# Performance work log

Measured on AMD Instinct MI355X. Metric: run time of the kernel, lower is better.

Reference implementation:

```python
import jax, jax.numpy as jnp
import numpy as np

L = 8        # path length (number of visited nodes)
N = 32768    # neighbors per node (fixed fan-out)
H = 404      # relation_dim == GRU hidden size
D = 128      # node_encode_dim
F = 532      # neighbor feature = D + H
SCALE = 0.05


def setup_inputs() -> dict:
    key = jax.random.key(0)
    ks = jax.random.split(key, 14)
    return {
        "query": jax.random.normal(ks[0], (1, H), jnp.float32),
        "path_nodes": jax.random.normal(ks[1], (L, D), jnp.float32),
        "neighbors": jax.random.normal(ks[2], (L, N, F), jnp.float32),
        "action_ids": jax.random.randint(ks[3], (L - 1,), 0, N),
        "W_ih": jax.random.normal(ks[4], (3 * H, 3 * D), jnp.float32) * SCALE,
        "W_hh": jax.random.normal(ks[5], (3 * H, H), jnp.float32) * SCALE,
        "b_ih": jax.random.normal(ks[6], (3 * H,), jnp.float32) * SCALE,
        "b_hh": jax.random.normal(ks[7], (3 * H,), jnp.float32) * SCALE,
        "W_fa": jax.random.normal(ks[8], (D, F), jnp.float32) * SCALE,
        "b_fa": jax.random.normal(ks[9], (D,), jnp.float32) * SCALE,
        "W_fs": jax.random.normal(ks[10], (D, H), jnp.float32) * SCALE,
        "b_fs": jax.random.normal(ks[11], (D,), jnp.float32) * SCALE,
        "W_fp": jax.random.normal(ks[12], (1, 2 * D), jnp.float32) * SCALE,
        "b_fp": jax.random.normal(ks[13], (1,), jnp.float32) * SCALE,
    }


def gru_cell(x, h, W_ih, W_hh, b_ih, b_hh):
    # torch.nn.GRUCell semantics; x: (1, 3D), h: (1, H)
    gi = x @ W_ih.T + b_ih   # (1, 3H)
    gh = h @ W_hh.T + b_hh   # (1, 3H)
    i_r, i_z, i_n = jnp.split(gi, 3, axis=-1)
    h_r, h_z, h_n = jnp.split(gh, 3, axis=-1)
    r = jax.nn.sigmoid(i_r + h_r)
    z = jax.nn.sigmoid(i_z + h_z)
    n = jnp.tanh(i_n + r * h_n)
    return (1.0 - z) * n + z * h


def reference(query, path_nodes, neighbors, action_ids,
              W_ih, W_hh, b_ih, b_hh, W_fa, b_fa, W_fs, b_fs, W_fp, b_fp):
    # FA over all hops' neighbor blocks at once: (L, N, F) x (D, F) -> (L, N, D)
    hnts = jnp.einsum('lnf,df->lnd', neighbors, W_fa) + b_fa
    hmax = jnp.max(hnts, axis=1)                        # (L, D)  column-wise max (== _Max)
    hsel = hnts[jnp.arange(L - 1), action_ids]          # (L-1, D) chosen-action rows

    # initial GRU step: cat(zeros, zeros, first node emb) with query as hidden
    x0 = jnp.concatenate([jnp.zeros((1, 2 * D), query.dtype), path_nodes[0:1]], axis=1)
    qt = gru_cell(x0, query, W_ih, W_hh, b_ih, b_hh)

    def step(qt, inp):
        hAt, hat, nxt = inp                             # each (D,)
        x = jnp.concatenate([hAt, hat, nxt])[None, :]   # (1, 3D)
        return gru_cell(x, qt, W_ih, W_hh, b_ih, b_hh), None

    qt, _ = jax.lax.scan(step, qt, (hmax[:-1], hsel, path_nodes[1:]))

    hSt = qt @ W_fs.T + b_fs                            # (1, D)
    u0 = jnp.concatenate([hSt, hmax[-1:]], axis=1) @ W_fp.T + b_fp   # (1, 1)
    uks = hSt @ hnts[-1].T                              # (1, N)
    return jax.nn.softmax(jnp.concatenate([u0, uks], axis=1), axis=1)
```

## Files before the change

kernel.cpp:

```cpp
#include <hip/hip_runtime.h>
#include <math.h>

#define L 8
#define N 32768
#define H 404
#define D 128
#define F 532
#define KT 9
#define GRU_BLOCKS 101

typedef __attribute__((ext_vector_type(8))) _Float16 half8;
typedef __attribute__((ext_vector_type(4))) float f32x4;
typedef __attribute__((address_space(3))) unsigned int as3_u32;
typedef __attribute__((address_space(1))) unsigned int as1_u32;

#define WS_WH2     0
#define WS_HMAXK   (WS_WH2 + 36864)
#define WS_HSEL    (WS_HMAXK + L * D)
#define WS_GI      (WS_HSEL + (L - 1) * D)
#define WS_HBUF    (WS_GI + L * 3 * H)
#define WS_HS      (WS_HBUF + 2 * H)
#define WS_SCAL    (WS_HS + D)
#define WS_CNT     (WS_SCAL + 4)
#define WS_PM      (WS_CNT + 4)
#define WS_PS      (WS_PM + 256)
#define WS_LOGITS  (WS_PS + 256)

__device__ __forceinline__ unsigned encf(float f) {
    unsigned u = __float_as_uint(f);
    return (u & 0x80000000u) ? ~u : (u | 0x80000000u);
}
__device__ __forceinline__ float decf(unsigned u) {
    unsigned b = (u & 0x80000000u) ? (u ^ 0x80000000u) : ~u;
    return __uint_as_float(b);
}
__device__ __forceinline__ float sigmoidf_(float x) {
    return 1.0f / (1.0f + __expf(-x));
}
__device__ __forceinline__ unsigned pk_f16(float a, float b) {
    auto h = __builtin_amdgcn_cvt_pkrtz(a, b);
    return *(unsigned*)&h;
}
__device__ __forceinline__ half8 pack8(float4 x0, float4 x1) {
    uint4 u = { pk_f16(x0.x, x0.y), pk_f16(x0.z, x0.w),
                pk_f16(x1.x, x1.y), pk_f16(x1.z, x1.w) };
    return *(half8*)&u;
}
__device__ __forceinline__ void gld16(const void* g, void* l) {
    __builtin_amdgcn_global_load_lds((const as1_u32*)g, (as3_u32*)l, 16, 0, 0);
}
__device__ __forceinline__ float aload(const float* p) {
    return __hip_atomic_load(p, __ATOMIC_RELAXED, __HIP_MEMORY_SCOPE_AGENT);
}
__device__ __forceinline__ void astore(float* p, float v) {
    __hip_atomic_store(p, v, __ATOMIC_RELAXED, __HIP_MEMORY_SCOPE_AGENT);
}

__global__ void k_prep(const float* __restrict__ Wfa, unsigned short* __restrict__ wh2,
                       unsigned* __restrict__ keys, unsigned* __restrict__ cnt) {
    int i = blockIdx.x * 256 + threadIdx.x;
    if (i < L * D) keys[i] = 0u;
    if (i == 2000) *cnt = 0u;
    if (i >= KT * 128 * 8) return;
    int kt = i / (128 * 8);
    int rem = i - kt * 128 * 8;
    int c = rem >> 3, j = rem & 7;
    int k0 = kt * 64 + (j ^ (c & 7)) * 8;
    unsigned short v[8];
#pragma unroll
    for (int e = 0; e < 8; ++e) {
        int k = k0 + e;
        float x = (k < F) ? Wfa[c * F + k] : 0.0f;
        _Float16 h = (_Float16)x;
        v[e] = *(unsigned short*)&h;
    }
    *(uint4*)(wh2 + (long)i * 8) = *(uint4*)v;
}

template<int HOP7>
__global__ __launch_bounds__(256, 3)
void k_big(const float* __restrict__ nb, const unsigned short* __restrict__ wh2,
           const float* __restrict__ bfa, const int* __restrict__ aid,
           unsigned* __restrict__ hmaxk, float* __restrict__ hsel,
           const float* __restrict__ hs_ws, float* __restrict__ logits,
           float* __restrict__ pm, float* __restrict__ ps) {
    __shared__ float As[128 * 64];
    __shared__ unsigned short Bs[128 * 64];
    __shared__ float sm2[2], ss2[2];

    const int bid = blockIdx.x;
    const int l_hop = HOP7 ? 7 : (bid >> 8);
    const int row0 = HOP7 ? bid * 128 : (bid & 255) * 128;
    const int tid = threadIdx.x;
    const int lane = tid & 63, w = tid >> 6;
    const int wm = w >> 1, wn = w & 1;
    const int lr = lane & 15, kg = lane >> 4;

    const float* xbase = nb + ((long)l_hop * N + row0) * F;

    f32x4 acc[4][4];
    float bv[4];
#pragma unroll
    for (int n = 0; n < 4; ++n) bv[n] = bfa[wn * 64 + n * 16 + lr];
#pragma unroll
    for (int m = 0; m < 4; ++m)
#pragma unroll
        for (int n = 0; n < 4; ++n) {
            acc[m][n][0] = bv[n]; acc[m][n][1] = bv[n];
            acc[m][n][2] = bv[n]; acc[m][n][3] = bv[n];
        }

    const int srow = lane >> 4;
    const int scp  = lane & 15;

    for (int kt = 0; kt < KT; ++kt) {
        const int fc = kt * 64;
        __syncthreads();
#pragma unroll
        for (int it = 0; it < 8; ++it) {
            int rbase = it * 16 + w * 4;
            int row = rbase + srow;
            int cg = scp ^ (row & 7);
            int col0 = fc + cg * 4;
            const float* src = xbase + (long)row * F + ((col0 < F) ? col0 : 0);
            gld16(src, (char*)As + rbase * 256);
        }
#pragma unroll
        for (int it = 0; it < 4; ++it) {
            int rb = it * 32 + w * 8;
            const char* src = (const char*)wh2 + (long)kt * 16384 + rb * 128 + lane * 16;
            gld16(src, (char*)Bs + rb * 128);
        }
        __syncthreads();

#pragma unroll
        for (int ks = 0; ks < 2; ++ks) {
            half8 b[4];
#pragma unroll
            for (int n = 0; n < 4; ++n) {
                int col = wn * 64 + n * 16 + lr;
                int ch = (ks * 4 + kg) ^ (col & 7);
                b[n] = *(const half8*)((const char*)Bs + col * 128 + ch * 16);
            }
#pragma unroll
            for (int m = 0; m < 4; ++m) {
                int row = wm * 64 + m * 16 + lr;
                int c0 = ks * 8 + kg * 2;
                const char* base = (const char*)As + row * 256;
                float4 x0 = *(const float4*)(base + (((c0)     ^ (row & 7)) << 4));
                float4 x1 = *(const float4*)(base + (((c0 + 1) ^ (row & 7)) << 4));
                half8 a = pack8(x0, x1);
#pragma unroll
                for (int n = 0; n < 4; ++n)
                    acc[m][n] = __builtin_amdgcn_mfma_f32_16x16x32_f16(a, b[n], acc[m][n], 0, 0, 0);
            }
        }
    }

    __syncthreads();

    if (!HOP7) {
        int br = aid[l_hop] - row0;
        if (br >= 0 && br < 128 && (br >> 6) == wm && ((br >> 2) & 3) == kg) {
            int msel = (br >> 4) & 3, rsel = br & 3;
#pragma unroll
            for (int n = 0; n < 4; ++n) {
                float vsel = 0.f;
#pragma unroll
                for (int m = 0; m < 4; ++m)
#pragma unroll
                    for (int r = 0; r < 4; ++r)
                        if (m == msel && r == rsel) vsel = acc[m][n][r];
                hsel[l_hop * D + wn * 64 + n * 16 + lr] = vsel;
            }
        }
    } else {
        float hsv[4];
#pragma unroll
        for (int n = 0; n < 4; ++n) hsv[n] = hs_ws[wn * 64 + n * 16 + lr];
        float p[4][4];
#pragma unroll
        for (int m = 0; m < 4; ++m)
#pragma unroll
            for (int r = 0; r < 4; ++r) {
                float s = hsv[0] * acc[m][0][r];
                s = fmaf(hsv[1], acc[m][1][r], s);
                s = fmaf(hsv[2], acc[m][2][r], s);
                s = fmaf(hsv[3], acc[m][3][r], s);
#pragma unroll
                for (int off = 1; off < 16; off <<= 1)
                    s += __shfl_xor(s, off, 64);
                p[m][r] = s;
            }
        float* part = (float*)As;
        if (lr == 0) {
#pragma unroll
            for (int m = 0; m < 4; ++m)
#pragma unroll
                for (int r = 0; r < 4; ++r)
                    part[wn * 128 + wm * 64 + m * 16 + kg * 4 + r] = p[m][r];
        }
        __syncthreads();
        float val = -3.4e38f, sv = 0.f;
        if (tid < 128) {
            val = part[tid] + part[128 + tid];
            logits[1 + row0 + tid] = val;
            sv = 1.0f;
        }
        float mv = val;
        for (int off = 1; off < 64; off <<= 1) {
            float m2 = __shfl_xor(mv, off, 64);
            float s2 = __shfl_xor(sv, off, 64);
            float M = fmaxf(mv, m2);
            sv = sv * __expf(mv - M) + s2 * __expf(m2 - M);
            mv = M;
        }
        if (lane == 0 && w < 2) { sm2[w] = mv; ss2[w] = sv; }
        __syncthreads();
        if (tid == 0) {
            float M = fmaxf(sm2[0], sm2[1]);
            float S = ss2[0] * __expf(sm2[0] - M) + ss2[1] * __expf(sm2[1] - M);
            pm[bid] = M; ps[bid] = S;
        }
        __syncthreads();
    }

    float cmax[4];
#pragma unroll
    for (int n = 0; n < 4; ++n) {
        float m0 = acc[0][n][0];
#pragma unroll
        for (int m = 0; m < 4; ++m)
#pragma unroll
            for (int r = 0; r < 4; ++r) m0 = fmaxf(m0, acc[m][n][r]);
        m0 = fmaxf(m0, __shfl_xor(m0, 16, 64));
        m0 = fmaxf(m0, __shfl_xor(m0, 32, 64));
        cmax[n] = m0;
    }
    float* wmaxp = (float*)As;
    if (kg == 0) {
#pragma unroll
        for (int n = 0; n < 4; ++n)
            wmaxp[wm * 128 + wn * 64 + n * 16 + lr] = cmax[n];
    }
    __syncthreads();
    if (tid < 128) {
        float mval = fmaxf(wmaxp[tid], wmaxp[128 + tid]);
        atomicMax(&hmaxk[l_hop * D + tid], encf(mval));
    }
}

__global__ void k_gi(const float* __restrict__ Wih, const float* __restrict__ bih,
                     const float* __restrict__ pn, const unsigned* __restrict__ hmaxk,
                     const float* __restrict__ hsel, float* __restrict__ gi) {
    __shared__ float xs[L][3 * D];
    const int tid = threadIdx.x;
    for (int i = tid; i < L * 3 * D; i += 256) {
        int t = i / (3 * D), k = i % (3 * D);
        float x;
        if (t == 0) {
            x = (k < 2 * D) ? 0.0f : pn[k - 2 * D];
        } else {
            if (k < D)            x = decf(hmaxk[(t - 1) * D + k]);
            else if (k < 2 * D)   x = hsel[(t - 1) * D + (k - D)];
            else                  x = pn[t * D + (k - 2 * D)];
        }
        xs[t][k] = x;
    }
    __syncthreads();

    const int lane = tid & 63;
    const int row = blockIdx.x * 4 + (tid >> 6);
    const float* wr = Wih + (long)row * 3 * D;
    float s[L];
#pragma unroll
    for (int t = 0; t < L; ++t) s[t] = 0.f;
#pragma unroll
    for (int c = 0; c < 6; ++c) {
        int k = lane + c * 64;
        float wv = wr[k];
#pragma unroll
        for (int t = 0; t < L; ++t) s[t] = fmaf(wv, xs[t][k], s[t]);
    }
#pragma unroll
    for (int t = 0; t < L; ++t)
        for (int off = 1; off < 64; off <<= 1) s[t] += __shfl_xor(s[t], off, 64);
    if (lane == 0) {
        float b = bih[row];
#pragma unroll
        for (int t = 0; t < L; ++t) gi[t * 3 * H + row] = s[t] + b;
    }
}

__global__ __launch_bounds__(256, 1)
void k_gru(const float* __restrict__ Whh, const float* __restrict__ bhh,
           const float* __restrict__ gi, const float* __restrict__ query,
           const float* __restrict__ Wfs, const float* __restrict__ bfs,
           float* __restrict__ hbuf, float* __restrict__ hs_ws,
           unsigned* __restrict__ cnt) {
    const int tid = threadIdx.x;
    const int lane = tid & 63;
    const int bid = blockIdx.x;
    const int j = bid * 4 + (tid >> 6);

    float wr[7], wz[7], wnn[7];
#pragma unroll
    for (int c = 0; c < 7; ++c) {
        int i = lane + c * 64;
        bool ok = i < H;
        wr[c]  = ok ? Whh[(long)j * H + i]           : 0.f;
        wz[c]  = ok ? Whh[(long)(H + j) * H + i]     : 0.f;
        wnn[c] = ok ? Whh[(long)(2 * H + j) * H + i] : 0.f;
    }
    float b_r = 0.f, b_z = 0.f, b_n = 0.f;
    if (lane == 0) { b_r = bhh[j]; b_z = bhh[H + j]; b_n = bhh[2 * H + j]; }

    for (int t = 0; t < L; ++t) {
        const float* hin = (t == 0) ? query : (hbuf + ((t - 1) & 1) * H);
        float* hout = hbuf + (t & 1) * H;
        float pr = 0.f, pz = 0.f, pn2 = 0.f;
#pragma unroll
        for (int c = 0; c < 7; ++c) {
            int i = lane + c * 64;
            float hv = 0.f;
            if (i < H) hv = (t == 0) ? hin[i] : aload(hin + i);
            pr  = fmaf(wr[c],  hv, pr);
            pz  = fmaf(wz[c],  hv, pz);
            pn2 = fmaf(wnn[c], hv, pn2);
        }
        for (int off = 1; off < 64; off <<= 1) {
            pr  += __shfl_xor(pr, off, 64);
            pz  += __shfl_xor(pz, off, 64);
            pn2 += __shfl_xor(pn2, off, 64);
        }
        if (lane == 0) {
            const float* gt = gi + t * 3 * H;
            float hprev = (t == 0) ? hin[j] : aload(hin + j);
            float r  = sigmoidf_(gt[j] + pr + b_r);
            float z  = sigmoidf_(gt[H + j] + pz + b_z);
            float nn = tanhf(gt[2 * H + j] + r * (pn2 + b_n));
            astore(hout + j, (1.0f - z) * nn + z * hprev);
        }
        __syncthreads();
        if (tid == 0) {
            __hip_atomic_fetch_add(cnt, 1u, __ATOMIC_RELEASE,
                                   __HIP_MEMORY_SCOPE_AGENT);
            unsigned target = (unsigned)GRU_BLOCKS * (t + 1);
            while (__hip_atomic_load(cnt, __ATOMIC_ACQUIRE,
                                     __HIP_MEMORY_SCOPE_AGENT) < target)
                __builtin_amdgcn_s_sleep(2);
        }
        __syncthreads();
    }

    if (bid < 32) {
        const float* qt = hbuf + H;
        int d = bid * 4 + (tid >> 6);
        float s = 0.f;
#pragma unroll
        for (int c = 0; c < 7; ++c) {
            int i = lane + c * 64;
            if (i < H) s = fmaf(aload(qt + i), Wfs[(long)d * H + i], s);
        }
        for (int off = 1; off < 64; off <<= 1) s += __shfl_xor(s, off, 64);
        if (lane == 0) astore(&hs_ws[d], s + bfs[d]);
    }
}

__global__ void k_sm12(const float* __restrict__ hs_ws, const float* __restrict__ Wfp,
                       const float* __restrict__ bfp, const unsigned* __restrict__ hmaxk,
                       const float* __restrict__ pm, const float* __restrict__ ps,
                       float* __restrict__ logits, float* __restrict__ scal) {
    __shared__ float red[4], reds[4], u0sh;
    int tid = threadIdx.x, lane = tid & 63, wid = tid >> 6;
    if (tid < 64) {
        float s = hs_ws[tid] * Wfp[tid];
        s = fmaf(hs_ws[tid + 64], Wfp[tid + 64], s);
        s = fmaf(decf(hmaxk[(L - 1) * D + tid]),      Wfp[D + tid],      s);
        s = fmaf(decf(hmaxk[(L - 1) * D + tid + 64]), Wfp[D + tid + 64], s);
        for (int off = 1; off < 64; off <<= 1) s += __shfl_xor(s, off, 64);
        if (tid == 0) { u0sh = s + bfp[0]; logits[0] = u0sh; }
    }
    __syncthreads();
    float m = -3.4e38f, s = 0.f;
    if (tid < 256) { m = pm[tid]; s = ps[tid]; }
    for (int off = 1; off < 64; off <<= 1) {
        float m2 = __shfl_xor(m, off, 64);
        float s2 = __shfl_xor(s, off, 64);
        float M = fmaxf(m, m2);
        s = s * __expf(m - M) + s2 * __expf(m2 - M);
        m = M;
    }
    if (lane == 0 && wid < 4) { red[wid] = m; reds[wid] = s; }
    __syncthreads();
    if (tid == 0) {
        float M = u0sh, S = 1.0f;
        for (int k = 0; k < 4; ++k) {
            float Mn = fmaxf(M, red[k]);
            S = S * __expf(M - Mn) + reds[k] * __expf(red[k] - Mn);
            M = Mn;
        }
        scal[1] = M; scal[2] = S;
    }
}

__global__ void k_sm3(const float* __restrict__ logits, const float* __restrict__ scal,
                      float* __restrict__ out) {
    int i = blockIdx.x * 256 + threadIdx.x;
    if (i <= N) out[i] = __expf(logits[i] - scal[1]) / scal[2];
}

extern "C" void kernel_launch(void* const* d_in, const int* in_sizes, int n_in,
                              void* d_out, int out_size, void* d_ws, size_t ws_size,
                              hipStream_t stream) {
    const float* query = (const float*)d_in[0];
    const float* pn    = (const float*)d_in[1];
    const float* nb    = (const float*)d_in[2];
    const int*   aid   = (const int*)d_in[3];
    const float* Wih   = (const float*)d_in[4];
    const float* Whh   = (const float*)d_in[5];
    const float* bih   = (const float*)d_in[6];
    const float* bhh   = (const float*)d_in[7];
    const float* Wfa   = (const float*)d_in[8];
    const float* bfa   = (const float*)d_in[9];
    const float* Wfs   = (const float*)d_in[10];
    const float* bfs   = (const float*)d_in[11];
    const float* Wfp   = (const float*)d_in[12];
    const float* bfp   = (const float*)d_in[13];

    float* ws = (float*)d_ws;
    unsigned short* wh2   = (unsigned short*)(ws + WS_WH2);
    unsigned*       hmaxk = (unsigned*)(ws + WS_HMAXK);
    unsigned*       cnt   = (unsigned*)(ws + WS_CNT);
    float* hsel   = ws + WS_HSEL;
    float* gi     = ws + WS_GI;
    float* hbuf   = ws + WS_HBUF;
    float* hs_ws  = ws + WS_HS;
    float* scal   = ws + WS_SCAL;
    float* pm     = ws + WS_PM;
    float* psum   = ws + WS_PS;
    float* logits = ws + WS_LOGITS;
    float* out    = (float*)d_out;

    k_prep<<<(KT * 128 * 8 + 255) / 256, 256, 0, stream>>>(Wfa, wh2, hmaxk, cnt);
    k_big<0><<<(L - 1) * 256, 256, 0, stream>>>(nb, wh2, bfa, aid, hmaxk, hsel,
                                                hs_ws, logits, pm, psum);
    k_gi  <<<303, 256, 0, stream>>>(Wih, bih, pn, hmaxk, hsel, gi);
    k_gru <<<GRU_BLOCKS, 256, 0, stream>>>(Whh, bhh, gi, query, Wfs, bfs,
                                           hbuf, hs_ws, cnt);
    k_big<1><<<256, 256, 0, stream>>>(nb, wh2, bfa, aid, hmaxk, hsel,
                                      hs_ws, logits, pm, psum);
    k_sm12<<<1, 1024, 0, stream>>>(hs_ws, Wfp, bfp, hmaxk, pm, psum, logits, scal);
    k_sm3 <<<(N + 1 + 255) / 256, 256, 0, stream>>>(logits, scal, out);
}
```

Before: 195.1 us.

## Overlap GRU recurrence with hop GEMMs via per-hop completion counters in one kernel

Merges the hop 0-6 GEMM blocks, the input-gate projection and the GRU recurrence into a single launch. The first 101 blocks run the GRU chain and spin on per-hop counters that the GEMM blocks bump when they finish, so each GRU step can start as soon as its hop's max and selected row are ready. The gi precompute kernel is dropped and the W_ih products are computed inline per step with weights held in registers. This saves two launches and lets the sequential GRU overlap the bandwidth-bound GEMM. In exchange, co-residency of the spinning chain blocks is required (lower block ids are assumed scheduled first), and those blocks occupy compute units during the GEMM.

```diff
diff --git a/kernel.cpp b/kernel.cpp
--- a/kernel.cpp
+++ b/kernel.cpp
@@ -7,7 +7,7 @@
 #define D 128
 #define F 532
 #define KT 9
-#define GRU_BLOCKS 101
+#define CHAINB 101
 
 typedef __attribute__((ext_vector_type(8))) _Float16 half8;
 typedef __attribute__((ext_vector_type(4))) float f32x4;
@@ -17,12 +17,11 @@
 #define WS_WH2     0
 #define WS_HMAXK   (WS_WH2 + 36864)
 #define WS_HSEL    (WS_HMAXK + L * D)
-#define WS_GI      (WS_HSEL + (L - 1) * D)
-#define WS_HBUF    (WS_GI + L * 3 * H)
+#define WS_HBUF    (WS_HSEL + (L - 1) * D)
 #define WS_HS      (WS_HBUF + 2 * H)
 #define WS_SCAL    (WS_HS + D)
 #define WS_CNT     (WS_SCAL + 4)
-#define WS_PM      (WS_CNT + 4)
+#define WS_PM      (WS_CNT + 16)
 #define WS_PS      (WS_PM + 256)
 #define WS_LOGITS  (WS_PS + 256)
 
@@ -52,15 +51,18 @@
 __device__ __forceinline__ float aload(const float* p) {
     return __hip_atomic_load(p, __ATOMIC_RELAXED, __HIP_MEMORY_SCOPE_AGENT);
 }
+__device__ __forceinline__ unsigned aloadu(const unsigned* p) {
+    return __hip_atomic_load(p, __ATOMIC_RELAXED, __HIP_MEMORY_SCOPE_AGENT);
+}
 __device__ __forceinline__ void astore(float* p, float v) {
     __hip_atomic_store(p, v, __ATOMIC_RELAXED, __HIP_MEMORY_SCOPE_AGENT);
 }
 
 __global__ void k_prep(const float* __restrict__ Wfa, unsigned short* __restrict__ wh2,
-                       unsigned* __restrict__ keys, unsigned* __restrict__ cnt) {
+                       unsigned* __restrict__ keys, unsigned* __restrict__ cnts) {
     int i = blockIdx.x * 256 + threadIdx.x;
     if (i < L * D) keys[i] = 0u;
-    if (i == 2000) *cnt = 0u;
+    if (i >= 2000 && i < 2016) cnts[i - 2000] = 0u;
     if (i >= KT * 128 * 8) return;
     int kt = i / (128 * 8);
     int rem = i - kt * 128 * 8;
@@ -77,22 +79,131 @@
     *(uint4*)(wh2 + (long)i * 8) = *(uint4*)v;
 }
 
-template<int HOP7>
 __global__ __launch_bounds__(256, 3)
-void k_big(const float* __restrict__ nb, const unsigned short* __restrict__ wh2,
-           const float* __restrict__ bfa, const int* __restrict__ aid,
-           unsigned* __restrict__ hmaxk, float* __restrict__ hsel,
-           const float* __restrict__ hs_ws, float* __restrict__ logits,
-           float* __restrict__ pm, float* __restrict__ ps) {
+void k_main(const float* __restrict__ nb, const unsigned short* __restrict__ wh2,
+            const float* __restrict__ bfa, const int* __restrict__ aid,
+            const float* __restrict__ pn, const float* __restrict__ query,
+            const float* __restrict__ Wih, const float* __restrict__ bih,
+            const float* __restrict__ Whh, const float* __restrict__ bhh,
+            const float* __restrict__ Wfs, const float* __restrict__ bfs,
+            unsigned* __restrict__ hmaxk, float* __restrict__ hsel,
+            float* __restrict__ hbuf, float* __restrict__ hs_ws,
+            unsigned* __restrict__ cnts) {
     __shared__ float As[128 * 64];
     __shared__ unsigned short Bs[128 * 64];
-    __shared__ float sm2[2], ss2[2];
 
     const int bid = blockIdx.x;
-    const int l_hop = HOP7 ? 7 : (bid >> 8);
-    const int row0 = HOP7 ? bid * 128 : (bid & 255) * 128;
     const int tid = threadIdx.x;
     const int lane = tid & 63, w = tid >> 6;
+    unsigned* cntG = cnts + 1;
+    unsigned* hopcnt = cnts + 3;
+
+    if (bid < CHAINB) {
+        float* xs = As;
+        const int j = bid * 4 + w;
+        float wir[6], wiz[6], win[6];
+#pragma unroll
+        for (int c = 0; c < 6; ++c) {
+            int k = lane + c * 64;
+            wir[c] = Wih[(long)j * 384 + k];
+            wiz[c] = Wih[(long)(H + j) * 384 + k];
+            win[c] = Wih[(long)(2 * H + j) * 384 + k];
+        }
+        float whr[7], whz[7], whn[7];
+#pragma unroll
+        for (int c = 0; c < 7; ++c) {
+            int i = lane + c * 64;
+            bool ok = i < H;
+            whr[c] = ok ? Whh[(long)j * H + i]           : 0.f;
+            whz[c] = ok ? Whh[(long)(H + j) * H + i]     : 0.f;
+            whn[c] = ok ? Whh[(long)(2 * H + j) * H + i] : 0.f;
+        }
+        const float b_ir = bih[j], b_iz = bih[H + j], b_in = bih[2 * H + j];
+        const float b_hr = bhh[j], b_hz = bhh[H + j], b_hn = bhh[2 * H + j];
+
+        for (int t = 0; t < L; ++t) {
+            if (t > 0) {
+                __syncthreads();
+                if (tid == 0) {
+                    while (__hip_atomic_load(hopcnt + (t - 1), __ATOMIC_ACQUIRE,
+                                             __HIP_MEMORY_SCOPE_AGENT) < 256u)
+                        __builtin_amdgcn_s_sleep(8);
+                }
+                __syncthreads();
+            }
+            for (int i = tid; i < 384; i += 256) {
+                float x;
+                if (t == 0)       x = (i < 256) ? 0.f : pn[i - 256];
+                else if (i < 128) x = decf(aloadu(hmaxk + (t - 1) * D + i));
+                else if (i < 256) x = aload(hsel + (t - 1) * D + (i - 128));
+                else              x = pn[t * D + (i - 256)];
+                xs[i] = x;
+            }
+            __syncthreads();
+            float gir = 0.f, giz = 0.f, gin = 0.f;
+#pragma unroll
+            for (int c = 0; c < 6; ++c) {
+                float xv = xs[lane + c * 64];
+                gir = fmaf(wir[c], xv, gir);
+                giz = fmaf(wiz[c], xv, giz);
+                gin = fmaf(win[c], xv, gin);
+            }
+            const float* hin = (t == 0) ? query : (hbuf + ((t - 1) & 1) * H);
+            float pr = 0.f, pz = 0.f, pn2 = 0.f;
+#pragma unroll
+            for (int c = 0; c < 7; ++c) {
+                int i = lane + c * 64;
+                float hv = 0.f;
+                if (i < H) hv = (t == 0) ? hin[i] : aload(hin + i);
+                pr  = fmaf(whr[c], hv, pr);
+                pz  = fmaf(whz[c], hv, pz);
+                pn2 = fmaf(whn[c], hv, pn2);
+            }
+            for (int off = 1; off < 64; off <<= 1) {
+                gir += __shfl_xor(gir, off, 64);
+                giz += __shfl_xor(giz, off, 64);
+                gin += __shfl_xor(gin, off, 64);
+                pr  += __shfl_xor(pr, off, 64);
+                pz  += __shfl_xor(pz, off, 64);
+                pn2 += __shfl_xor(pn2, off, 64);
+            }
+            if (lane == 0) {
+                float* hout = hbuf + (t & 1) * H;
+                float hprev = (t == 0) ? hin[j] : aload(hin + j);
+                float r  = sigmoidf_((gir + b_ir) + pr + b_hr);
+                float z  = sigmoidf_((giz + b_iz) + pz + b_hz);
+                float nn = tanhf((gin + b_in) + r * (pn2 + b_hn));
+                astore(hout + j, (1.0f - z) * nn + z * hprev);
+            }
+            __syncthreads();
+            if (tid == 0) {
+                __hip_atomic_fetch_add(cntG, 1u, __ATOMIC_RELEASE,
+                                       __HIP_MEMORY_SCOPE_AGENT);
+                unsigned target = (unsigned)CHAINB * (t + 1);
+                while (__hip_atomic_load(cntG, __ATOMIC_ACQUIRE,
+                                         __HIP_MEMORY_SCOPE_AGENT) < target)
+                    __builtin_amdgcn_s_sleep(2);
+            }
+            __syncthreads();
+        }
+        if (bid < 32) {
+            const float* qt = hbuf + H;
+            int d = bid * 4 + w;
+            float s = 0.f;
+#pragma unroll
+            for (int c = 0; c < 7; ++c) {
+                int i = lane + c * 64;
+                if (i < H) s = fmaf(aload(qt + i), Wfs[(long)d * H + i], s);
+            }
+            for (int off = 1; off < 64; off <<= 1) s += __shfl_xor(s, off, 64);
+            if (lane == 0) astore(&hs_ws[d], s + bfs[d]);
+        }
+        return;
+    }
+
+    const int idx = bid - CHAINB;
+    const int l_hop = idx >> 8;
+    const int row0 = (idx & 255) * 128;
     const int wm = w >> 1, wn = w & 1;
     const int lr = lane & 15, kg = lane >> 4;
 
@@ -159,7 +270,7 @@
 
     __syncthreads();
 
-    if (!HOP7) {
+    {
         int br = aid[l_hop] - row0;
         if (br >= 0 && br < 128 && (br >> 6) == wm && ((br >> 2) & 3) == kg) {
             int msel = (br >> 4) & 3, rsel = br & 3;
@@ -171,58 +282,9 @@
 #pragma unroll
                     for (int r = 0; r < 4; ++r)
                         if (m == msel && r == rsel) vsel = acc[m][n][r];
-                hsel[l_hop * D + wn * 64 + n * 16 + lr] = vsel;
-            }
-        }
-    } else {
-        float hsv[4];
-#pragma unroll
-        for (int n = 0; n < 4; ++n) hsv[n] = hs_ws[wn * 64 + n * 16 + lr];
-        float p[4][4];
-#pragma unroll
-        for (int m = 0; m < 4; ++m)
-#pragma unroll
-            for (int r = 0; r < 4; ++r) {
-                float s = hsv[0] * acc[m][0][r];
-                s = fmaf(hsv[1], acc[m][1][r], s);
-                s = fmaf(hsv[2], acc[m][2][r], s);
-                s = fmaf(hsv[3], acc[m][3][r], s);
-#pragma unroll
-                for (int off = 1; off < 16; off <<= 1)
-                    s += __shfl_xor(s, off, 64);
-                p[m][r] = s;
-            }
-        float* part = (float*)As;
-        if (lr == 0) {
-#pragma unroll
-            for (int m = 0; m < 4; ++m)
-#pragma unroll
-                for (int r = 0; r < 4; ++r)
-                    part[wn * 128 + wm * 64 + m * 16 + kg * 4 + r] = p[m][r];
-        }
-        __syncthreads();
-        float val = -3.4e38f, sv = 0.f;
-        if (tid < 128) {
-            val = part[tid] + part[128 + tid];
-            logits[1 + row0 + tid] = val;
-            sv = 1.0f;
-        }
-        float mv = val;
-        for (int off = 1; off < 64; off <<= 1) {
-            float m2 = __shfl_xor(mv, off, 64);
-            float s2 = __shfl_xor(sv, off, 64);
-            float M = fmaxf(mv, m2);
-            sv = sv * __expf(mv - M) + s2 * __expf(m2 - M);
-            mv = M;
-        }
-        if (lane == 0 && w < 2) { sm2[w] = mv; ss2[w] = sv; }
-        __syncthreads();
-        if (tid == 0) {
-            float M = fmaxf(sm2[0], sm2[1]);
-            float S = ss2[0] * __expf(sm2[0] - M) + ss2[1] * __expf(sm2[1] - M);
-            pm[bid] = M; ps[bid] = S;
-        }
-        __syncthreads();
+                astore(&hsel[l_hop * D + wn * 64 + n * 16 + lr], vsel);
+            }
+        }
     }
 
     float cmax[4];
@@ -248,122 +310,162 @@
         float mval = fmaxf(wmaxp[tid], wmaxp[128 + tid]);
         atomicMax(&hmaxk[l_hop * D + tid], encf(mval));
     }
-}
-
-__global__ void k_gi(const float* __restrict__ Wih, const float* __restrict__ bih,
-                     const float* __restrict__ pn, const unsigned* __restrict__ hmaxk,
-                     const float* __restrict__ hsel, float* __restrict__ gi) {
-    __shared__ float xs[L][3 * D];
+    __syncthreads();
+    if (tid == 0)
+        __hip_atomic_fetch_add(hopcnt + l_hop, 1u, __ATOMIC_RELEASE,
+                               __HIP_MEMORY_SCOPE_AGENT);
+}
+
+__global__ __launch_bounds__(256, 3)
+void k_big7(const float* __restrict__ nb, const unsigned short* __restrict__ wh2,
+            const float* __restrict__ bfa, unsigned* __restrict__ hmaxk,
+            const float* __restrict__ hs_ws, float* __restrict__ logits,
+            float* __restrict__ pm, float* __restrict__ ps) {
+    __shared__ float As[128 * 64];
+    __shared__ unsigned short Bs[128 * 64];
+    __shared__ float sm2[2], ss2[2];
+
+    const int bid = blockIdx.x;
+    const int row0 = bid * 128;
     const int tid = threadIdx.x;
-    for (int i = tid; i < L * 3 * D; i += 256) {
-        int t = i / (3 * D), k = i % (3 * D);
-        float x;
-        if (t == 0) {
-            x = (k < 2 * D) ? 0.0f : pn[k - 2 * D];
-        } else {
-            if (k < D)            x = decf(hmaxk[(t - 1) * D + k]);
-            else if (k < 2 * D)   x = hsel[(t - 1) * D + (k - D)];
-            else                  x = pn[t * D + (k - 2 * D)];
-        }
-        xs[t][k] = x;
-    }
-    __syncthreads();
-
-    const int lane = tid & 63;
-    const int row = blockIdx.x * 4 + (tid >> 6);
-    const float* wr = Wih + (long)row * 3 * D;
-    float s[L];
-#pragma unroll
-    for (int t = 0; t < L; ++t) s[t] = 0.f;
-#pragma unroll
-    for (int c = 0; c < 6; ++c) {
-        int k = lane + c * 64;
-        float wv = wr[k];
-#pragma unroll
-        for (int t = 0; t < L; ++t) s[t] = fmaf(wv, xs[t][k], s[t]);
-    }
-#pragma unroll
-    for (int t = 0; t < L; ++t)
-        for (int off = 1; off < 64; off <<= 1) s[t] += __shfl_xor(s[t], off, 64);
-    if (lane == 0) {
-        float b = bih[row];
-#pragma unroll
-        for (int t = 0; t < L; ++t) gi[t * 3 * H + row] = s[t] + b;
-    }
-}
-
-__global__ __launch_bounds__(256, 1)
-void k_gru(const float* __restrict__ Whh, const float* __restrict__ bhh,
-           const float* __restrict__ gi, const float* __restrict__ query,
-           const float* __restrict__ Wfs, const float* __restrict__ bfs,
-           float* __restrict__ hbuf, float* __restrict__ hs_ws,
-           unsigned* __restrict__ cnt) {
-    const int tid = threadIdx.x;
-    const int lane = tid & 63;
-    const int bid = blockIdx.x;
-    const int j = bid * 4 + (tid >> 6);
-
-    float wr[7], wz[7], wnn[7];
-#pragma unroll
-    for (int c = 0; c < 7; ++c) {
-        int i = lane + c * 64;
-        bool ok = i < H;
-        wr[c]  = ok ? Whh[(long)j * H + i]           : 0.f;
-        wz[c]  = ok ? Whh[(long)(H + j) * H + i]     : 0.f;
-        wnn[c] = ok ? Whh[(long)(2 * H + j) * H + i] : 0.f;
-    }
-    float b_r = 0.f, b_z = 0.f, b_n = 0.f;
-    if (lane == 0) { b_r = bhh[j]; b_z = bhh[H + j]; b_n = bhh[2 * H + j]; }
-
-    for (int t = 0; t < L; ++t) {
-        const float* hin = (t == 0) ? query : (hbuf + ((t - 1) & 1) * H);
-        float* hout = hbuf + (t & 1) * H;
-        float pr = 0.f, pz = 0.f, pn2 = 0.f;
-#pragma unroll
-        for (int c = 0; c < 7; ++c) {
-            int i = lane + c * 64;
-            float hv = 0.f;
-            if (i < H) hv = (t == 0) ? hin[i] : aload(hin + i);
-            pr  = fmaf(wr[c],  hv, pr);
-            pz  = fmaf(wz[c],  hv, pz);
-            pn2 = fmaf(wnn[c], hv, pn2);
-        }
-        for (int off = 1; off < 64; off <<= 1) {
-            pr  += __shfl_xor(pr, off, 64);
-            pz  += __shfl_xor(pz, off, 64);
-            pn2 += __shfl_xor(pn2, off, 64);
-        }
-        if (lane == 0) {
-            const float* gt = gi + t * 3 * H;
-            float hprev = (t == 0) ? hin[j] : aload(hin + j);
-            float r  = sigmoidf_(gt[j] + pr + b_r);
-            float z  = sigmoidf_(gt[H + j] + pz + b_z);
-            float nn = tanhf(gt[2 * H + j] + r * (pn2 + b_n));
-            astore(hout + j, (1.0f - z) * nn + z * hprev);
-        }
+    const int lane = tid & 63, w = tid >> 6;
+    const int wm = w >> 1, wn = w & 1;
+    const int lr = lane & 15, kg = lane >> 4;
+
+    const float* xbase = nb + ((long)7 * N + row0) * F;
+
+    f32x4 acc[4][4];
+    float bv[4];
+#pragma unroll
+    for (int n = 0; n < 4; ++n) bv[n] = bfa[wn * 64 + n * 16 + lr];
+#pragma unroll
+    for (int m = 0; m < 4; ++m)
+#pragma unroll
+        for (int n = 0; n < 4; ++n) {
+            acc[m][n][0] = bv[n]; acc[m][n][1] = bv[n];
+            acc[m][n][2] = bv[n]; acc[m][n][3] = bv[n];
+        }
+
+    const int srow = lane >> 4;
+    const int scp  = lane & 15;
+
+    for (int kt = 0; kt < KT; ++kt) {
+        const int fc = kt * 64;
         __syncthreads();
-        if (tid == 0) {
-            __hip_atomic_fetch_add(cnt, 1u, __ATOMIC_RELEASE,
-                                   __HIP_MEMORY_SCOPE_AGENT);
-            unsigned target = (unsigned)GRU_BLOCKS * (t + 1);
-            while (__hip_atomic_load(cnt, __ATOMIC_ACQUIRE,
-                                     __HIP_MEMORY_SCOPE_AGENT) < target)
-                __builtin_amdgcn_s_sleep(2);
+#pragma unroll
+        for (int it = 0; it < 8; ++it) {
+            int rbase = it * 16 + w * 4;
+            int row = rbase + srow;
+            int cg = scp ^ (row & 7);
+            int col0 = fc + cg * 4;
+            const float* src = xbase + (long)row * F + ((col0 < F) ? col0 : 0);
+            gld16(src, (char*)As + rbase * 256);
+        }
+#pragma unroll
+        for (int it = 0; it < 4; ++it) {
+            int rb = it * 32 + w * 8;
+            const char* src = (const char*)wh2 + (long)kt * 16384 + rb * 128 + lane * 16;
+            gld16(src, (char*)Bs + rb * 128);
         }
         __syncthreads();
-    }
-
-    if (bid < 32) {
-        const float* qt = hbuf + H;
-        int d = bid * 4 + (tid >> 6);
-        float s = 0.f;
-#pragma unroll
-        for (int c = 0; c < 7; ++c) {
-            int i = lane + c * 64;
-            if (i < H) s = fmaf(aload(qt + i), Wfs[(long)d * H + i], s);
-        }
-        for (int off = 1; off < 64; off <<= 1) s += __shfl_xor(s, off, 64);
-        if (lane == 0) astore(&hs_ws[d], s + bfs[d]);
+
+#pragma unroll
+        for (int ks = 0; ks < 2; ++ks) {
+            half8 b[4];
+#pragma unroll
+            for (int n = 0; n < 4; ++n) {
+                int col = wn * 64 + n * 16 + lr;
+                int ch = (ks * 4 + kg) ^ (col & 7);
+                b[n] = *(const half8*)((const char*)Bs + col * 128 + ch * 16);
+            }
+#pragma unroll
+            for (int m = 0; m < 4; ++m) {
+                int row = wm * 64 + m * 16 + lr;
+                int c0 = ks * 8 + kg * 2;
+                const char* base = (const char*)As + row * 256;
+                float4 x0 = *(const float4*)(base + (((c0)     ^ (row & 7)) << 4));
+                float4 x1 = *(const float4*)(base + (((c0 + 1) ^ (row & 7)) << 4));
+                half8 a = pack8(x0, x1);
+#pragma unroll
+                for (int n = 0; n < 4; ++n)
+                    acc[m][n] = __builtin_amdgcn_mfma_f32_16x16x32_f16(a, b[n], acc[m][n], 0, 0, 0);
+            }
+        }
+    }
+
+    __syncthreads();
+
+    float hsv[4];
+#pragma unroll
+    for (int n = 0; n < 4; ++n) hsv[n] = hs_ws[wn * 64 + n * 16 + lr];
+    float p[4][4];
+#pragma unroll
+    for (int m = 0; m < 4; ++m)
+#pragma unroll
+        for (int r = 0; r < 4; ++r) {
+            float s = hsv[0] * acc[m][0][r];
+            s = fmaf(hsv[1], acc[m][1][r], s);
+            s = fmaf(hsv[2], acc[m][2][r], s);
+            s = fmaf(hsv[3], acc[m][3][r], s);
+#pragma unroll
+            for (int off = 1; off < 16; off <<= 1)
+                s += __shfl_xor(s, off, 64);
+            p[m][r] = s;
+        }
+    float* part = (float*)As;
+    if (lr == 0) {
+#pragma unroll
+        for (int m = 0; m < 4; ++m)
+#pragma unroll
+            for (int r = 0; r < 4; ++r)
+                part[wn * 128 + wm * 64 + m * 16 + kg * 4 + r] = p[m][r];
+    }
+    __syncthreads();
+    float val = -3.4e38f, sv = 0.f;
+    if (tid < 128) {
+        val = part[tid] + part[128 + tid];
+        logits[1 + row0 + tid] = val;
+        sv = 1.0f;
+    }
+    float mv = val;
+    for (int off = 1; off < 64; off <<= 1) {
+        float m2 = __shfl_xor(mv, off, 64);
+        float s2 = __shfl_xor(sv, off, 64);
+        float M = fmaxf(mv, m2);
+        sv = sv * __expf(mv - M) + s2 * __expf(m2 - M);
+        mv = M;
+    }
+    if (lane == 0 && w < 2) { sm2[w] = mv; ss2[w] = sv; }
+    __syncthreads();
+    if (tid == 0) {
+        float M = fmaxf(sm2[0], sm2[1]);
+        float S = ss2[0] * __expf(sm2[0] - M) + ss2[1] * __expf(sm2[1] - M);
+        pm[bid] = M; ps[bid] = S;
+    }
+    __syncthreads();
+
+    float cmax[4];
+#pragma unroll
+    for (int n = 0; n < 4; ++n) {
+        float m0 = acc[0][n][0];
+#pragma unroll
+        for (int m = 0; m < 4; ++m)
+#pragma unroll
+            for (int r = 0; r < 4; ++r) m0 = fmaxf(m0, acc[m][n][r]);
+        m0 = fmaxf(m0, __shfl_xor(m0, 16, 64));
+        m0 = fmaxf(m0, __shfl_xor(m0, 32, 64));
+        cmax[n] = m0;
+    }
+    float* wmaxp = (float*)As;
+    if (kg == 0) {
+#pragma unroll
+        for (int n = 0; n < 4; ++n)
+            wmaxp[wm * 128 + wn * 64 + n * 16 + lr] = cmax[n];
+    }
+    __syncthreads();
+    if (tid < 128) {
+        float mval = fmaxf(wmaxp[tid], wmaxp[128 + tid]);
+        atomicMax(&hmaxk[7 * D + tid], encf(mval));
     }
 }
 
@@ -431,9 +533,8 @@
     float* ws = (float*)d_ws;
     unsigned short* wh2   = (unsigned short*)(ws + WS_WH2);
     unsigned*       hmaxk = (unsigned*)(ws + WS_HMAXK);
-    unsigned*       cnt   = (unsigned*)(ws + WS_CNT);
+    unsigned*       cnts  = (unsigned*)(ws + WS_CNT);
     float* hsel   = ws + WS_HSEL;
-    float* gi     = ws + WS_GI;
     float* hbuf   = ws + WS_HBUF;
     float* hs_ws  = ws + WS_HS;
     float* scal   = ws + WS_SCAL;
@@ -442,14 +543,11 @@
     float* logits = ws + WS_LOGITS;
     float* out    = (float*)d_out;
 
-    k_prep<<<(KT * 128 * 8 + 255) / 256, 256, 0, stream>>>(Wfa, wh2, hmaxk, cnt);
-    k_big<0><<<(L - 1) * 256, 256, 0, stream>>>(nb, wh2, bfa, aid, hmaxk, hsel,
-                                                hs_ws, logits, pm, psum);
-    k_gi  <<<303, 256, 0, stream>>>(Wih, bih, pn, hmaxk, hsel, gi);
-    k_gru <<<GRU_BLOCKS, 256, 0, stream>>>(Whh, bhh, gi, query, Wfs, bfs,
-                                           hbuf, hs_ws, cnt);
-    k_big<1><<<256, 256, 0, stream>>>(nb, wh2, bfa, aid, hmaxk, hsel,
-                                      hs_ws, logits, pm, psum);
+    k_prep<<<(KT * 128 * 8 + 255) / 256, 256, 0, stream>>>(Wfa, wh2, hmaxk, cnts);
+    k_main<<<CHAINB + 7 * 256, 256, 0, stream>>>(nb, wh2, bfa, aid, pn, query,
+                                                 Wih, bih, Whh, bhh, Wfs, bfs,
+                                                 hmaxk, hsel, hbuf, hs_ws, cnts);
+    k_big7<<<256, 256, 0, stream>>>(nb, wh2, bfa, hmaxk, hs_ws, logits, pm, psum);
     k_sm12<<<1, 1024, 0, stream>>>(hs_ws, Wfp, bfp, hmaxk, pm, psum, logits, scal);
     k_sm3 <<<(N + 1 + 255) / 256, 256, 0, stream>>>(logits, scal, out);
 }
```

Result: slower. 343.2 us (+75.9%).
